# Performance work log

Hardware: AMD Instinct MI355X
Metric: run time of the kernel (lower is better)

The kernel has to match this reference:

```python
import jax, jax.numpy as jnp
import numpy as np

V = 100000
E = 1600000
IN_CH = 128
HEADS = 4
OUT_CH = 16
NEG_SLOPE = 0.2


def setup_inputs() -> dict:
    key = jax.random.key(0)
    k1, k2, k3, k4, k5 = jax.random.split(key, 5)
    x = jax.random.normal(k1, (V, IN_CH), dtype=jnp.float32)
    edge_index = jax.random.randint(k2, (2, E), 0, V, dtype=jnp.int32)
    # Xavier-ish scaled params
    W = jax.random.normal(k3, (IN_CH, HEADS * OUT_CH), dtype=jnp.float32) / np.sqrt(IN_CH)
    a_src = jax.random.normal(k4, (HEADS, OUT_CH), dtype=jnp.float32) / np.sqrt(OUT_CH)
    a_dst = jax.random.normal(k5, (HEADS, OUT_CH), dtype=jnp.float32) / np.sqrt(OUT_CH)
    return {"x": x, "edge_index": edge_index, "W": W, "a_src": a_src, "a_dst": a_dst}


def reference(x, edge_index, W, a_src, a_dst):
    v = x.shape[0]
    h, cout = a_src.shape
    z = (x @ W).reshape(v, h, cout)                      # [V,H,C]
    src, dst = edge_index[0], edge_index[1]
    # per-node attention logits, then gather at edges (same math as gather-then-dot)
    e_src = jnp.einsum("vhc,hc->vh", z, a_src)           # [V,H]
    e_dst = jnp.einsum("vhc,hc->vh", z, a_dst)           # [V,H]
    e = jax.nn.leaky_relu(e_src[src] + e_dst[dst], NEG_SLOPE)  # [E,H]
    # scatter softmax over dst per head
    m = jax.ops.segment_max(e, dst, num_segments=v)      # [V,H]
    # nodes with no incoming edges get -inf max; edges never reference them
    exp_e = jnp.exp(e - m[dst])                          # [E,H]
    denom = jax.ops.segment_sum(exp_e, dst, num_segments=v)  # [V,H]
    alpha = exp_e / (denom[dst] + 1e-9)                  # [E,H]
    # scatter aggregation of weighted source features
    agg = jax.ops.segment_sum(z[src] * alpha[:, :, None], dst, num_segments=v)  # [V,H,C]
    out = jax.nn.elu(agg)
    return out.reshape(v, h * cout)
```

## Files before the change

### kernel.cpp

```cpp
#include <hip/hip_runtime.h>
#include <hip/hip_bf16.h>
#include <cstdint>

#define NV 100000
#define NE 1600000
#define KIN 128
#define NH 4
#define NC 16
#define NF 64
#define NBKT 1563
#define BCAP 1216
#define EPW 8
#define BINWG 391
#define GEMMWG 782
#define XSTR 136

typedef __attribute__((ext_vector_type(8))) short bf16x8;
typedef __attribute__((ext_vector_type(4))) float f32x4;

__device__ __forceinline__ short f2bf(float f) {
    unsigned u = __float_as_uint(f);
    return (short)((u + 0x7FFFu + ((u >> 16) & 1u)) >> 16);
}

__device__ __forceinline__ unsigned enc11(float w) {
    unsigned t = (__float_as_uint(w) + 0x10000u) >> 17;
    t = min(max(t, 7168u), 9215u);
    return t - 7168u;
}

__global__ __launch_bounds__(256) void k_prep(
    const float* __restrict__ W, const float* __restrict__ a_src,
    const float* __restrict__ a_dst, short* __restrict__ wfrag,
    int* __restrict__ gcur)
{
    const int g = blockIdx.x * 256 + threadIdx.x;
    if (g < NBKT) gcur[g] = 0;
    if (g < 1280) {
        const int lane = g & 63;
        const int ctks = g >> 6;
        const int ct = ctks >> 2, ks = ctks & 3;
        const int n = lane & 15, quad = lane >> 4;
        short* dst = wfrag + (size_t)g * 8;
#pragma unroll
        for (int j = 0; j < 8; ++j) {
            const int k = ks * 32 + quad * 8 + j;
            float v = 0.f;
            if (ct < 4) {
                v = W[k * NF + ct * 16 + n];
            } else if (n < 8) {
                const int h = n & 3;
                const float* __restrict__ a =
                    (n < 4) ? (a_src + h * 16) : (a_dst + h * 16);
                for (int c = 0; c < 16; ++c)
                    v += W[k * NF + h * 16 + c] * a[c];
            }
            dst[j] = f2bf(v);
        }
    }
}

__global__ __launch_bounds__(512) void k_front(
    const float* __restrict__ x, const short* __restrict__ wfrag,
    __hip_bfloat16* __restrict__ z, float* __restrict__ esrc,
    float* __restrict__ edst,
    const int* __restrict__ ei, int* __restrict__ gcur,
    unsigned* __restrict__ barr)
{
    __shared__ union SM {
        struct { int hist[NBKT]; int base[NBKT]; } bin;
        short xs[128 * XSTR];
    } sm;

    const int bi = blockIdx.x;
    const bool isbin = (bi < 2 * BINWG) && !(bi & 1);
    const int id = (bi < 2 * BINWG) ? (bi >> 1) : (bi - BINWG);

    if (isbin) {
        int* hist = sm.bin.hist;
        int* base = sm.bin.base;
        const int t = threadIdx.x;
        const int e0 = id * (512 * EPW);

        for (int i = t; i < NBKT; i += 512) hist[i] = 0;
        __syncthreads();

        unsigned pk[EPW];
        short bk[EPW];
#pragma unroll
        for (int i = 0; i < EPW; ++i) {
            const int e = e0 + i * 512 + t;
            if (e < NE) {
                const int s = ei[e];
                const int d = ei[NE + e];
                const int bkt = d >> 6;
                bk[i] = (short)bkt;
                pk[i] = ((unsigned)(d & 63) << 17) | (unsigned)s;
                atomicAdd(&hist[bkt], 1);
            } else {
                bk[i] = -1;
            }
        }
        __syncthreads();
        for (int i = t; i < NBKT; i += 512) {
            const int c = hist[i];
            base[i] = c ? atomicAdd(&gcur[i], c) : 0;
            hist[i] = 0;
        }
        __syncthreads();
#pragma unroll
        for (int i = 0; i < EPW; ++i) {
            if (bk[i] >= 0) {
                const int bkt = bk[i];
                const int pos = base[bkt] + atomicAdd(&hist[bkt], 1);
                if (pos < BCAP)
                    barr[(size_t)bkt * BCAP + pos] = pk[i];
            }
        }
    } else {
        short* xs = sm.xs;
        const int t = threadIdx.x;
        const float4* __restrict__ x4 = (const float4*)x;

#pragma unroll
        for (int i = 0; i < 8; ++i) {
            const int li = i * 512 + t;
            const int idx = id * 4096 + li;
            float4 v = make_float4(0.f, 0.f, 0.f, 0.f);
            if (idx < NV * (KIN / 4)) v = x4[idx];
            const unsigned lo = (unsigned)(unsigned short)f2bf(v.x)
                              | ((unsigned)(unsigned short)f2bf(v.y) << 16);
            const unsigned hi = (unsigned)(unsigned short)f2bf(v.z)
                              | ((unsigned)(unsigned short)f2bf(v.w) << 16);
            *(uint2*)&xs[(li >> 5) * XSTR + (li & 31) * 4] = make_uint2(lo, hi);
        }
        __syncthreads();

        const int wv = t >> 6;
        const int lane = t & 63;
        const int n = lane & 15;
        const int quad = lane >> 4;

        bf16x8 bf[20];
        const bf16x8* __restrict__ wf = (const bf16x8*)wfrag;
#pragma unroll
        for (int i = 0; i < 20; ++i) bf[i] = wf[i * 64 + lane];

        const short* __restrict__ arow = &xs[(wv * 16 + n) * XSTR];
        f32x4 acc[5];
#pragma unroll
        for (int ct = 0; ct < 5; ++ct) acc[ct] = (f32x4){0.f, 0.f, 0.f, 0.f};

#pragma unroll
        for (int ks = 0; ks < 4; ++ks) {
            const bf16x8 af = *(const bf16x8*)(arow + ks * 32 + quad * 8);
#pragma unroll
            for (int ct = 0; ct < 5; ++ct)
                acc[ct] = __builtin_amdgcn_mfma_f32_16x16x32_bf16(
                    af, bf[ct * 4 + ks], acc[ct], 0, 0, 0);
        }

        unsigned short* __restrict__ zz = (unsigned short*)z;
#pragma unroll
        for (int ct = 0; ct < 4; ++ct) {
#pragma unroll
            for (int reg = 0; reg < 4; ++reg) {
                const int r_g = id * 128 + wv * 16 + quad * 4 + reg;
                if (r_g < NV)
                    zz[(size_t)r_g * NF + ct * 16 + n] =
                        (unsigned short)f2bf(acc[ct][reg]);
            }
        }
#pragma unroll
        for (int reg = 0; reg < 4; ++reg) {
            const int r_g = id * 128 + wv * 16 + quad * 4 + reg;
            if (r_g < NV && n < 8) {
                const float v = acc[4][reg];
                if (n < 4) esrc[r_g * NH + n] = v;
                else       edst[r_g * NH + (n - 4)] = v;
            }
        }
    }
}

__global__ __launch_bounds__(256) void k_back(
    const int* __restrict__ gcur, const unsigned* __restrict__ barr,
    const float* __restrict__ esrc, const float* __restrict__ edst,
    const __hip_bfloat16* __restrict__ z, float* __restrict__ out)
{
    __shared__ __align__(16) unsigned arr[BCAP];
    __shared__ unsigned long long rec[BCAP];
    __shared__ int hist[64], off[64], cur[64];
    __shared__ float4 led[64];
    const int t = threadIdx.x;
    const int b = blockIdx.x;
    int f = gcur[b]; if (f > BCAP) f = BCAP;
    const unsigned* __restrict__ bp = barr + (size_t)b * BCAP;

    if (t < 64) {
        hist[t] = 0;
        cur[t] = 0;
        const int d = b * 64 + t;
        led[t] = (d < NV) ? *(const float4*)(edst + (size_t)d * 4)
                          : make_float4(0.f, 0.f, 0.f, 0.f);
    }
    __syncthreads();
    const int f4 = f >> 2;
    for (int i = t; i < f4; i += 256) {
        const uint4 v = ((const uint4*)bp)[i];
        ((uint4*)arr)[i] = v;
        atomicAdd(&hist[v.x >> 17], 1);
        atomicAdd(&hist[v.y >> 17], 1);
        atomicAdd(&hist[v.z >> 17], 1);
        atomicAdd(&hist[v.w >> 17], 1);
    }
    for (int i = (f4 << 2) + t; i < f; i += 256) {
        const unsigned v = bp[i];
        arr[i] = v;
        atomicAdd(&hist[v >> 17], 1);
    }
    __syncthreads();
    if (t < 64) off[t] = hist[t];
    __syncthreads();
    for (int s = 1; s < 64; s <<= 1) {
        const int v = (t < 64 && t >= s) ? off[t - s] : 0;
        __syncthreads();
        if (t < 64) off[t] += v;
        __syncthreads();
    }
    if (t < 64) off[t] -= hist[t];
    __syncthreads();

    for (int i = t; i < f; i += 256) {
        const unsigned p = arr[i];
        const int dl = p >> 17;
        const unsigned s = p & 0x1FFFFu;
        const int slot = off[dl] + atomicAdd(&cur[dl], 1);
        const float4 e4 = *(const float4*)(esrc + (size_t)s * 4);
        const float4 ed = led[dl];
        float ev;
        ev = e4.x + ed.x; ev = ev > 0.f ? ev : 0.2f * ev;
        const unsigned w0 = enc11(__expf(ev));
        ev = e4.y + ed.y; ev = ev > 0.f ? ev : 0.2f * ev;
        const unsigned w1 = enc11(__expf(ev));
        ev = e4.z + ed.z; ev = ev > 0.f ? ev : 0.2f * ev;
        const unsigned w2 = enc11(__expf(ev));
        ev = e4.w + ed.w; ev = ev > 0.f ? ev : 0.2f * ev;
        const unsigned w3 = enc11(__expf(ev));
        rec[slot] = (unsigned long long)s
            | ((unsigned long long)w0 << 17)
            | ((unsigned long long)w1 << 28)
            | ((unsigned long long)w2 << 39)
            | ((unsigned long long)w3 << 50);
    }
    __syncthreads();

    const int wv = t >> 6;
    const int lane = t & 63;
    const int quad = lane >> 4;
    const int li = lane & 15;
    const int sh = 17 + 11 * (li >> 2);
    const unsigned short* __restrict__ zb = (const unsigned short*)z + li * 4;

    for (int k = 0; k < 16; ++k) {
        const int dl = (k << 2) | wv;
        const int d = b * 64 + dl;
        const int begin = off[dl];
        const int nd = hist[dl];
        float a0 = 0.f, a1 = 0.f, a2 = 0.f, a3 = 0.f, den = 0.f;
        for (int j = 0; j < nd; j += 8) {
            const int je0 = j + quad;
            const int je1 = je0 + 4;
            const unsigned long long r0 = (je0 < nd) ? rec[begin + je0] : 0ull;
            const unsigned long long r1 = (je1 < nd) ? rec[begin + je1] : 0ull;
            const unsigned s0 = (unsigned)r0 & 0x1FFFFu;
            const unsigned s1 = (unsigned)r1 & 0x1FFFFu;
            const float w0 = __uint_as_float(
                ((((unsigned)(r0 >> sh)) & 0x7FFu) + 7168u) << 17);
            const float w1 = __uint_as_float(
                ((((unsigned)(r1 >> sh)) & 0x7FFu) + 7168u) << 17);
            const uint2 zv0 = *(const uint2*)(zb + ((size_t)s0 << 6));
            const uint2 zv1 = *(const uint2*)(zb + ((size_t)s1 << 6));
            a0 = fmaf(w0, __uint_as_float(zv0.x << 16), a0);
            a1 = fmaf(w0, __uint_as_float(zv0.x & 0xFFFF0000u), a1);
            a2 = fmaf(w0, __uint_as_float(zv0.y << 16), a2);
            a3 = fmaf(w0, __uint_as_float(zv0.y & 0xFFFF0000u), a3);
            den += w0;
            a0 = fmaf(w1, __uint_as_float(zv1.x << 16), a0);
            a1 = fmaf(w1, __uint_as_float(zv1.x & 0xFFFF0000u), a1);
            a2 = fmaf(w1, __uint_as_float(zv1.y << 16), a2);
            a3 = fmaf(w1, __uint_as_float(zv1.y & 0xFFFF0000u), a3);
            den += w1;
        }
        a0 += __shfl_xor(a0, 16); a0 += __shfl_xor(a0, 32);
        a1 += __shfl_xor(a1, 16); a1 += __shfl_xor(a1, 32);
        a2 += __shfl_xor(a2, 16); a2 += __shfl_xor(a2, 32);
        a3 += __shfl_xor(a3, 16); a3 += __shfl_xor(a3, 32);
        den += __shfl_xor(den, 16); den += __shfl_xor(den, 32);
        if (lane < 16 && d < NV) {
            const float id = 1.f / (den + 1e-9f);
            float v0 = a0 * id, v1 = a1 * id, v2 = a2 * id, v3 = a3 * id;
            v0 = v0 > 0.f ? v0 : __expf(v0) - 1.f;
            v1 = v1 > 0.f ? v1 : __expf(v1) - 1.f;
            v2 = v2 > 0.f ? v2 : __expf(v2) - 1.f;
            v3 = v3 > 0.f ? v3 : __expf(v3) - 1.f;
            *(float4*)(out + (size_t)d * NF + li * 4) =
                make_float4(v0, v1, v2, v3);
        }
    }
}

extern "C" void kernel_launch(void* const* d_in, const int* in_sizes, int n_in,
                              void* d_out, int out_size, void* d_ws, size_t ws_size,
                              hipStream_t stream)
{
    const float* x     = (const float*)d_in[0];
    const int*   ei    = (const int*)d_in[1];
    const float* W     = (const float*)d_in[2];
    const float* a_src = (const float*)d_in[3];
    const float* a_dst = (const float*)d_in[4];
    float* out = (float*)d_out;

    char* p = (char*)d_ws;
    __hip_bfloat16* z = (__hip_bfloat16*)p;  p += (size_t)NV * NF * 2;
    float* esrc = (float*)p;                 p += (size_t)NV * NH * 4;
    float* edst = (float*)p;                 p += (size_t)NV * NH * 4;
    int*   gcur = (int*)p;                   p += (size_t)NBKT * 4;
    p = (char*)(((uintptr_t)p + 255) & ~(uintptr_t)255);
    short* wfrag = (short*)p;                p += (size_t)1280 * 8 * 2;
    p = (char*)(((uintptr_t)p + 255) & ~(uintptr_t)255);
    unsigned* barr = (unsigned*)p;           p += (size_t)NBKT * BCAP * 4;

    k_prep<<<7, 256, 0, stream>>>(W, a_src, a_dst, wfrag, gcur);
    k_front<<<2 * BINWG + (GEMMWG - BINWG), 512, 0, stream>>>(
        x, wfrag, z, esrc, edst, ei, gcur, barr);
    k_back<<<NBKT, 256, 0, stream>>>(gcur, barr, esrc, edst, z, out);
}
```

Measured before the change: 180.1 us.

## Fold weight prep into front kernel and compute logits via shuffle reductions

Removes the separate prep kernel: each GEMM workgroup now loads and converts W to bf16 fragments directly from global memory, and the gcur reset moves to a memset. The attention logits are computed from the fp32 accumulators with per-16-lane shuffle reductions against a_src/a_dst instead of an extra MFMA column tile. Binning blocks now process 16 edges per thread and are interleaved one in five with GEMM blocks. This trades one kernel launch and one MFMA tile for redundant strided W loads in every GEMM block and extra shuffles.

```diff
diff --git a/kernel.cpp b/kernel.cpp
--- a/kernel.cpp
+++ b/kernel.cpp
@@ -10,9 +10,10 @@
 #define NF 64
 #define NBKT 1563
 #define BCAP 1216
-#define EPW 8
-#define BINWG 391
+#define EPW 16
+#define BINWG 196
 #define GEMMWG 782
+#define NITEMS 978
 #define XSTR 136
 
 typedef __attribute__((ext_vector_type(8))) short bf16x8;
@@ -29,39 +30,9 @@
     return t - 7168u;
 }
 
-__global__ __launch_bounds__(256) void k_prep(
-    const float* __restrict__ W, const float* __restrict__ a_src,
-    const float* __restrict__ a_dst, short* __restrict__ wfrag,
-    int* __restrict__ gcur)
-{
-    const int g = blockIdx.x * 256 + threadIdx.x;
-    if (g < NBKT) gcur[g] = 0;
-    if (g < 1280) {
-        const int lane = g & 63;
-        const int ctks = g >> 6;
-        const int ct = ctks >> 2, ks = ctks & 3;
-        const int n = lane & 15, quad = lane >> 4;
-        short* dst = wfrag + (size_t)g * 8;
-#pragma unroll
-        for (int j = 0; j < 8; ++j) {
-            const int k = ks * 32 + quad * 8 + j;
-            float v = 0.f;
-            if (ct < 4) {
-                v = W[k * NF + ct * 16 + n];
-            } else if (n < 8) {
-                const int h = n & 3;
-                const float* __restrict__ a =
-                    (n < 4) ? (a_src + h * 16) : (a_dst + h * 16);
-                for (int c = 0; c < 16; ++c)
-                    v += W[k * NF + h * 16 + c] * a[c];
-            }
-            dst[j] = f2bf(v);
-        }
-    }
-}
-
 __global__ __launch_bounds__(512) void k_front(
-    const float* __restrict__ x, const short* __restrict__ wfrag,
+    const float* __restrict__ x, const float* __restrict__ W,
+    const float* __restrict__ a_src, const float* __restrict__ a_dst,
     __hip_bfloat16* __restrict__ z, float* __restrict__ esrc,
     float* __restrict__ edst,
     const int* __restrict__ ei, int* __restrict__ gcur,
@@ -73,14 +44,12 @@
     } sm;
 
     const int bi = blockIdx.x;
-    const bool isbin = (bi < 2 * BINWG) && !(bi & 1);
-    const int id = (bi < 2 * BINWG) ? (bi >> 1) : (bi - BINWG);
-
-    if (isbin) {
+    const int t = threadIdx.x;
+
+    if (bi % 5 == 0) {
         int* hist = sm.bin.hist;
         int* base = sm.bin.base;
-        const int t = threadIdx.x;
-        const int e0 = id * (512 * EPW);
+        const int e0 = (bi / 5) * (512 * EPW);
 
         for (int i = t; i < NBKT; i += 512) hist[i] = 0;
         __syncthreads();
@@ -119,7 +88,7 @@
         }
     } else {
         short* xs = sm.xs;
-        const int t = threadIdx.x;
+        const int id = bi - bi / 5 - 1;
         const float4* __restrict__ x4 = (const float4*)x;
 
 #pragma unroll
@@ -141,43 +110,62 @@
         const int n = lane & 15;
         const int quad = lane >> 4;
 
-        bf16x8 bf[20];
-        const bf16x8* __restrict__ wf = (const bf16x8*)wfrag;
-#pragma unroll
-        for (int i = 0; i < 20; ++i) bf[i] = wf[i * 64 + lane];
+        bf16x8 bf[16];
+#pragma unroll
+        for (int ct = 0; ct < 4; ++ct) {
+#pragma unroll
+            for (int ks = 0; ks < 4; ++ks) {
+                bf16x8 f;
+#pragma unroll
+                for (int j = 0; j < 8; ++j) {
+                    const int k = ks * 32 + quad * 8 + j;
+                    f[j] = f2bf(W[k * NF + ct * 16 + n]);
+                }
+                bf[ct * 4 + ks] = f;
+            }
+        }
 
         const short* __restrict__ arow = &xs[(wv * 16 + n) * XSTR];
-        f32x4 acc[5];
-#pragma unroll
-        for (int ct = 0; ct < 5; ++ct) acc[ct] = (f32x4){0.f, 0.f, 0.f, 0.f};
+        f32x4 acc[4];
+#pragma unroll
+        for (int ct = 0; ct < 4; ++ct) acc[ct] = (f32x4){0.f, 0.f, 0.f, 0.f};
 
 #pragma unroll
         for (int ks = 0; ks < 4; ++ks) {
             const bf16x8 af = *(const bf16x8*)(arow + ks * 32 + quad * 8);
 #pragma unroll
-            for (int ct = 0; ct < 5; ++ct)
+            for (int ct = 0; ct < 4; ++ct)
                 acc[ct] = __builtin_amdgcn_mfma_f32_16x16x32_bf16(
                     af, bf[ct * 4 + ks], acc[ct], 0, 0, 0);
         }
 
+        float as[4], ad[4];
+#pragma unroll
+        for (int ct = 0; ct < 4; ++ct) {
+            as[ct] = a_src[ct * 16 + n];
+            ad[ct] = a_dst[ct * 16 + n];
+        }
         unsigned short* __restrict__ zz = (unsigned short*)z;
 #pragma unroll
         for (int ct = 0; ct < 4; ++ct) {
 #pragma unroll
             for (int reg = 0; reg < 4; ++reg) {
                 const int r_g = id * 128 + wv * 16 + quad * 4 + reg;
-                if (r_g < NV)
-                    zz[(size_t)r_g * NF + ct * 16 + n] =
-                        (unsigned short)f2bf(acc[ct][reg]);
-            }
-        }
-#pragma unroll
-        for (int reg = 0; reg < 4; ++reg) {
-            const int r_g = id * 128 + wv * 16 + quad * 4 + reg;
-            if (r_g < NV && n < 8) {
-                const float v = acc[4][reg];
-                if (n < 4) esrc[r_g * NH + n] = v;
-                else       edst[r_g * NH + (n - 4)] = v;
+                const float v = acc[ct][reg];
+                float ps = v * as[ct];
+                float pd = v * ad[ct];
+#pragma unroll
+                for (int m = 8; m >= 1; m >>= 1) {
+                    ps += __shfl_xor(ps, m, 16);
+                    pd += __shfl_xor(pd, m, 16);
+                }
+                if (r_g < NV) {
+                    zz[(size_t)r_g * NF + ct * 16 + n] = (unsigned short)f2bf(v);
+                    if (n == 0) {
+                        esrc[r_g * NH + ct] = ps;
+                        edst[r_g * NH + ct] = pd;
+                    }
+                }
             }
         }
     }
@@ -327,12 +315,10 @@
     float* edst = (float*)p;                 p += (size_t)NV * NH * 4;
     int*   gcur = (int*)p;                   p += (size_t)NBKT * 4;
     p = (char*)(((uintptr_t)p + 255) & ~(uintptr_t)255);
-    short* wfrag = (short*)p;                p += (size_t)1280 * 8 * 2;
-    p = (char*)(((uintptr_t)p + 255) & ~(uintptr_t)255);
     unsigned* barr = (unsigned*)p;           p += (size_t)NBKT * BCAP * 4;
 
-    k_prep<<<7, 256, 0, stream>>>(W, a_src, a_dst, wfrag, gcur);
-    k_front<<<2 * BINWG + (GEMMWG - BINWG), 512, 0, stream>>>(
-        x, wfrag, z, esrc, edst, ei, gcur, barr);
+    hipMemsetAsync(gcur, 0, (size_t)NBKT * 4, stream);
+    k_front<<<NITEMS, 512, 0, stream>>>(x, W, a_src, a_dst, z, esrc, edst,
+                                        ei, gcur, barr);
     k_back<<<NBKT, 256, 0, stream>>>(gcur, barr, esrc, edst, z, out);
 }
```

Result: no change. 180.7 us (+0.3%).
